# Kernel optimization log

Measured on AMD Instinct MI355X. Metric: run time of the kernel, lower is better.

The kernel has to match this reference:

```python
import jax, jax.numpy as jnp
import numpy as np

DIM = 512
HEADS = 8
HD = DIM // HEADS

def _rotate_half(t):
    t1, t2 = jnp.split(t, 2, axis=-1)
    return jnp.concatenate((-t2, t1), axis=-1)

def _layernorm(x, g, b, eps=1e-5):
    mu = jnp.mean(x, axis=-1, keepdims=True)
    var = jnp.var(x, axis=-1, keepdims=True)
    return (x - mu) * jax.lax.rsqrt(var + eps) * g + b

def setup_inputs() -> dict:
    key = jax.random.key(0)
    ks = jax.random.split(key, 12)
    B, S = 4, 2048
    x = jax.random.normal(ks[0], (B, S, DIM), dtype=jnp.float32)
    rope_cos = jax.random.uniform(ks[1], (1, S, 1, HD), dtype=jnp.float32)
    rope_sin = jax.random.uniform(ks[2], (1, S, 1, HD), dtype=jnp.float32)
    sd = 1.0 / np.sqrt(DIM)
    params = {
        'norm1_g': jnp.ones((DIM,), jnp.float32),
        'norm1_b': jnp.zeros((DIM,), jnp.float32),
        'norm2_g': jnp.ones((DIM,), jnp.float32),
        'norm2_b': jnp.zeros((DIM,), jnp.float32),
        'w_qkv': jax.random.uniform(ks[3], (DIM, 3 * DIM), jnp.float32, -sd, sd),
        'b_qkv': jax.random.uniform(ks[4], (3 * DIM,), jnp.float32, -sd, sd),
        'w_proj': jax.random.uniform(ks[5], (DIM, DIM), jnp.float32, -sd, sd),
        'b_proj': jax.random.uniform(ks[6], (DIM,), jnp.float32, -sd, sd),
        'w_fc1': jax.random.uniform(ks[7], (DIM, 4 * DIM), jnp.float32, -sd, sd),
        'b_fc1': jax.random.uniform(ks[8], (4 * DIM,), jnp.float32, -sd, sd),
        'w_fc2': jax.random.uniform(ks[9], (4 * DIM, DIM), jnp.float32, -1.0 / np.sqrt(4 * DIM), 1.0 / np.sqrt(4 * DIM)),
        'b_fc2': jax.random.uniform(ks[10], (DIM,), jnp.float32, -1.0 / np.sqrt(4 * DIM), 1.0 / np.sqrt(4 * DIM)),
    }
    return {'x': x, 'rope_cos': rope_cos, 'rope_sin': rope_sin, **params}

def reference(x, rope_cos, rope_sin, norm1_g, norm1_b, norm2_g, norm2_b,
              w_qkv, b_qkv, w_proj, b_proj, w_fc1, b_fc1, w_fc2, b_fc2):
    B, S, D = x.shape
    scale = 1.0 / np.sqrt(HD)
    shortcut = x
    h = _layernorm(x, norm1_g, norm1_b)
    qkv = (h @ w_qkv + b_qkv).reshape(B, S, 3, HEADS, HD)
    q, k, v = qkv[:, :, 0], qkv[:, :, 1], qkv[:, :, 2]  # [B,S,H,hd]
    q = q * rope_cos + _rotate_half(q) * rope_sin
    k = k * rope_cos + _rotate_half(k) * rope_sin
    # attention over heads: scores [B,H,S,S]
    attn = jnp.einsum('bqhd,bkhd->bhqk', q, k) * scale
    attn = jax.nn.softmax(attn, axis=-1)
    o = jnp.einsum('bhqk,bkhd->bqhd', attn, v).reshape(B, S, D)
    o = o @ w_proj + b_proj
    x = shortcut + o  # dropout is identity in eval
    h2 = _layernorm(x, norm2_g, norm2_b)
    mlp = jax.nn.gelu(h2 @ w_fc1 + b_fc1, approximate=False) @ w_fc2 + b_fc2
    return x + mlp
```

## Files before the change

kernel.cpp:

```cpp
#include <hip/hip_runtime.h>
#include <cstdint>
#include <cstddef>

typedef unsigned short u16;
typedef unsigned int   u32;
typedef __bf16 bf16x8 __attribute__((ext_vector_type(8)));
typedef float  f32x4  __attribute__((ext_vector_type(4)));

#define BS   8192
#define DIMM 512
#define NH   8
#define HD   64
#define SEQ  2048
#define DFF  2048
#define NQKV 1536

#define GLD16(g, l) __builtin_amdgcn_global_load_lds( \
    (__attribute__((address_space(1))) const void*)(g), \
    (__attribute__((address_space(3))) void*)(l), 16, 0, 0)

__device__ __forceinline__ float b2f(u16 s) {
  u32 u = ((u32)s) << 16;
  float f; __builtin_memcpy(&f, &u, 4); return f;
}
__device__ __forceinline__ u16 f2b(float f) {
  u32 u; __builtin_memcpy(&u, &f, 4);
  u += 0x7fffu + ((u >> 16) & 1u);
  return (u16)(u >> 16);
}
__device__ __forceinline__ u16 f2b_rtz(float f) {
  u32 u; __builtin_memcpy(&u, &f, 4);
  return (u16)(u >> 16);
}

#define SZ_QKV (DIMM * NQKV)
#define SZ_PRJ (DIMM * DIMM)
#define SZ_F1  (DIMM * DFF)
#define SZ_F2  (DFF * DIMM)
__global__ __launch_bounds__(256) void transpose_all_k(
    const float* __restrict__ w_qkv, const float* __restrict__ w_prj,
    const float* __restrict__ w_f1,  const float* __restrict__ w_f2,
    u16* __restrict__ o_qkv, u16* __restrict__ o_prj,
    u16* __restrict__ o_f1,  u16* __restrict__ o_f2) {
  int idx = blockIdx.x * 256 + threadIdx.x;
  const float* W; u16* O; int Kd, Nd, off;
  if (idx < SZ_QKV)                         { W = w_qkv; O = o_qkv; Kd = DIMM; Nd = NQKV; off = idx; }
  else if (idx < SZ_QKV + SZ_PRJ)           { W = w_prj; O = o_prj; Kd = DIMM; Nd = DIMM; off = idx - SZ_QKV; }
  else if (idx < SZ_QKV + SZ_PRJ + SZ_F1)   { W = w_f1;  O = o_f1;  Kd = DIMM; Nd = DFF;  off = idx - SZ_QKV - SZ_PRJ; }
  else                                      { W = w_f2;  O = o_f2;  Kd = DFF;  Nd = DIMM; off = idx - SZ_QKV - SZ_PRJ - SZ_F1; }
  int n = off / Kd, k = off - n * Kd;
  O[off] = f2b(W[(size_t)k * Nd + n]);
}

__global__ __launch_bounds__(256) void ln_f32b_k(const float* __restrict__ X,
    const float* __restrict__ G, const float* __restrict__ Bb, u16* __restrict__ out) {
  int w = threadIdx.x >> 6, lane = threadIdx.x & 63;
  size_t row = (size_t)blockIdx.x * 4 + w;
  const float* xr = X + row * DIMM;
  float v[8];
  *(float4*)&v[0] = *(const float4*)(xr + lane * 8);
  *(float4*)&v[4] = *(const float4*)(xr + lane * 8 + 4);
  float s = 0.f, s2 = 0.f;
#pragma unroll
  for (int j = 0; j < 8; j++) { s += v[j]; s2 += v[j] * v[j]; }
#pragma unroll
  for (int m = 1; m < 64; m <<= 1) { s += __shfl_xor(s, m); s2 += __shfl_xor(s2, m); }
  float mu = s * (1.f / DIMM);
  float rsd = rsqrtf(s2 * (1.f / DIMM) - mu * mu + 1e-5f);
  float g[8], bb[8];
  *(float4*)&g[0]  = *(const float4*)(G + lane * 8);
  *(float4*)&g[4]  = *(const float4*)(G + lane * 8 + 4);
  *(float4*)&bb[0] = *(const float4*)(Bb + lane * 8);
  *(float4*)&bb[4] = *(const float4*)(Bb + lane * 8 + 4);
  uint4 ov; u16* os = (u16*)&ov;
#pragma unroll
  for (int j = 0; j < 8; j++) os[j] = f2b((v[j] - mu) * rsd * g[j] + bb[j]);
  *(uint4*)(out + row * DIMM + lane * 8) = ov;
}

template <int EPI, int TM, int TN, int BK>
__global__ __launch_bounds__(256) void gemm_bt(const u16* __restrict__ A,
    const u16* __restrict__ BT, const float* __restrict__ bias,
    void* __restrict__ Cout, const float* __restrict__ resid, int N, int Kd) {
  constexpr int CPR  = BK / 8;
  constexpr int CPRB = (BK == 64) ? 3 : 2;
  constexpr int RS   = (BK == 64) ? 0 : 1;
  constexpr int KK   = BK / 32;
  constexpr int WROWS = (TN == 128) ? TM / 2 : TM / 4;
  constexpr int MT   = WROWS / 16;
  __shared__ __align__(16) u16 a_s[2][TM * BK];
  __shared__ __align__(16) u16 b_s[2][TN * BK];
  int t = threadIdx.x, lane = t & 63, w = t >> 6;
  int l15 = lane & 15, quad = lane >> 4;
  int gx = gridDim.x;
  int lid = blockIdx.x + gx * blockIdx.y;
  int per = (gx * gridDim.y) >> 3;
  int nid = (lid & 7) * per + (lid >> 3);
  int bx = nid % gx, by = nid / gx;
  int m0 = by * TM, n0 = bx * TN;
  int wm = (TN == 128) ? (w >> 1) * WROWS : w * WROWS;
  int wn = (TN == 128) ? (w & 1) * 64 : 0;
  f32x4 z4 = {0.f, 0.f, 0.f, 0.f};
  f32x4 acc[MT][4];
#pragma unroll
  for (int i = 0; i < MT; i++)
#pragma unroll
    for (int j = 0; j < 4; j++) acc[i][j] = z4;

#define GSTAGE(buf, ts) do {                                                  \
    int k0_ = (ts) * BK;                                                      \
    _Pragma("unroll")                                                         \
    for (int i = 0; i < TM * CPR / 256; i++) {                                \
      int c_ = t + i * 256;                                                   \
      int row_ = c_ >> CPRB, pos_ = c_ & (CPR - 1);                           \
      int ch_ = (pos_ ^ (row_ >> RS)) & (CPR - 1);                            \
      GLD16(A + (size_t)(m0 + row_) * Kd + k0_ + ch_ * 8, &a_s[buf][c_ * 8]); \
    }                                                                         \
    _Pragma("unroll")                                                         \
    for (int i = 0; i < TN * CPR / 256; i++) {                                \
      int c_ = t + i * 256;                                                   \
      int row_ = c_ >> CPRB, pos_ = c_ & (CPR - 1);                           \
      int ch_ = (pos_ ^ (row_ >> RS)) & (CPR - 1);                            \
      GLD16(BT + (size_t)(n0 + row_) * Kd + k0_ + ch_ * 8, &b_s[buf][c_ * 8]);\
    }                                                                         \
  } while (0)

#define GCOMPUTE(buf) do {                                                    \
    bf16x8 af[MT][KK], bfm[4][KK];                                            \
    _Pragma("unroll")                                                         \
    for (int mt = 0; mt < MT; mt++) {                                         \
      _Pragma("unroll")                                                       \
      for (int kk = 0; kk < KK; kk++) {                                       \
        int row_ = wm + mt * 16 + l15;                                        \
        int pos_ = ((kk * 4 + quad) ^ (row_ >> RS)) & (CPR - 1);              \
        af[mt][kk] = *(const bf16x8*)&a_s[buf][row_ * BK + pos_ * 8];         \
      }                                                                       \
    }                                                                         \
    _Pragma("unroll")                                                         \
    for (int nt = 0; nt < 4; nt++) {                                          \
      _Pragma("unroll")                                                       \
      for (int kk = 0; kk < KK; kk++) {                                       \
        int row_ = wn + nt * 16 + l15;                                        \
        int pos_ = ((kk * 4 + quad) ^ (row_ >> RS)) & (CPR - 1);              \
        bfm[nt][kk] = *(const bf16x8*)&b_s[buf][row_ * BK + pos_ * 8];        \
      }                                                                       \
    }                                                                         \
    _Pragma("unroll")                                                         \
    for (int kk = 0; kk < KK; kk++)                                           \
      _Pragma("unroll")                                                       \
      for (int mt = 0; mt < MT; mt++)                                         \
        _Pragma("unroll")                                                     \
        for (int nt = 0; nt < 4; nt++)                                        \
          acc[mt][nt] = __builtin_amdgcn_mfma_f32_16x16x32_bf16(              \
              af[mt][kk], bfm[nt][kk], acc[mt][nt], 0, 0, 0);                 \
  } while (0)

  GSTAGE(0, 0);
  __syncthreads();
  int nsteps = Kd / BK;
  for (int ts = 0; ts < nsteps; ts += 2) {
    GSTAGE(1, ts + 1);
    GCOMPUTE(0);
    __syncthreads();
    if (ts + 2 < nsteps) GSTAGE(0, ts + 2);
    GCOMPUTE(1);
    __syncthreads();
  }
#undef GSTAGE
#undef GCOMPUTE

#pragma unroll
  for (int nt = 0; nt < 4; nt++) {
    int col = n0 + wn + nt * 16 + l15;
    float bv = bias[col];
#pragma unroll
    for (int mt = 0; mt < MT; mt++) {
#pragma unroll
      for (int r = 0; r < 4; r++) {
        int rw = m0 + wm + mt * 16 + quad * 4 + r;
        float v = acc[mt][nt][r] + bv;
        size_t off = (size_t)rw * N + col;
        if (EPI == 0) {
          ((float*)Cout)[off] = v;
        } else if (EPI == 1) {
          ((float*)Cout)[off] = v + resid[off];
        } else if (EPI == 2) {
          ((u16*)Cout)[off] = f2b(0.5f * v * (1.f + erff(v * 0.70710678118654752f)));
        } else {
          ((u16*)Cout)[off] = f2b(v);
        }
      }
    }
  }
}

#define QSCALE 0.18033688f
__global__ __launch_bounds__(256) void rope_k(const u16* __restrict__ qkv,
    const float* __restrict__ C, const float* __restrict__ Sn,
    u16* __restrict__ Qo, u16* __restrict__ Ko, u16* __restrict__ Vo) {
  int idx = blockIdx.x * 256 + threadIdx.x;
  int row = idx / 192;
  int cn = idx - row * 192;
  int n0 = cn * 8;
  int comp = n0 >> 9;
  int hh = (n0 >> 6) & 7;
  int d0 = n0 & 63;
  int b = row >> 11, s = row & 2047;
  const u16* src = qkv + (size_t)row * NQKV;
  uint4 val = *(const uint4*)(src + n0);
  u16* vs = (u16*)&val;
  size_t oo = ((size_t)((b << 3) + hh) * SEQ + s) * HD + d0;
  if (comp == 2) { *(uint4*)(Vo + oo) = val; return; }
  uint4 pv = *(const uint4*)(src + (n0 ^ 32));
  u16* ps = (u16*)&pv;
  float cv[8], sv[8];
  *(float4*)&cv[0] = *(const float4*)(C + s * HD + d0);
  *(float4*)&cv[4] = *(const float4*)(C + s * HD + d0 + 4);
  *(float4*)&sv[0] = *(const float4*)(Sn + s * HD + d0);
  *(float4*)&sv[4] = *(const float4*)(Sn + s * HD + d0 + 4);
  float sgn = (d0 & 32) ? 1.f : -1.f;
  float sc = (comp == 0) ? QSCALE : 1.f;
  uint4 ov; u16* os = (u16*)&ov;
#pragma unroll
  for (int j = 0; j < 8; j++)
    os[j] = f2b(sc * (b2f(vs[j]) * cv[j] + sgn * b2f(ps[j]) * sv[j]));
  *(uint4*)((comp == 0 ? Qo : Ko) + oo) = ov;
}

__global__ __launch_bounds__(256) void vtrans_k(const u16* __restrict__ V,
                                                u16* __restrict__ Vt) {
  __shared__ u16 ld[64 * 72];
  int t = threadIdx.x;
  int bh = blockIdx.x >> 5;
  int s0 = (blockIdx.x & 31) * 64;
  const u16* src = V + (size_t)bh * SEQ * HD + (size_t)s0 * HD;
  u16* dst = Vt + (size_t)bh * SEQ * HD;
#pragma unroll
  for (int i = 0; i < 2; i++) {
    int c = t + i * 256, s = c >> 3, cp = c & 7;
    *(uint4*)&ld[s * 72 + ((cp ^ (s >> 3)) << 3)] =
        *(const uint4*)(src + (size_t)s * HD + cp * 8);
  }
  __syncthreads();
#pragma unroll
  for (int i = 0; i < 2; i++) {
    int c = t + i * 256, d = c >> 3, sc = c & 7;
    uint4 ov; u16* os = (u16*)&ov;
#pragma unroll
    for (int j = 0; j < 8; j++) {
      int s = sc * 8 + j;
      os[j] = ld[s * 72 + (((d >> 3) ^ (s >> 3)) << 3) + (d & 7)];
    }
    *(uint4*)(dst + (size_t)d * SEQ + s0 + sc * 8) = ov;
  }
}

__global__ __launch_bounds__(512) void attn_flash_k(const u16* __restrict__ Qg,
    const u16* __restrict__ Kg, const u16* __restrict__ Vtg, u16* __restrict__ Og) {
  __shared__ u16 q_s[128 * 72];
  __shared__ u16 k_s[64 * 72];
  __shared__ u16 vt_s[64 * 72];
  int t = threadIdx.x, lane = t & 63, w = t >> 6;
  int l15 = lane & 15, quad = lane >> 4;
  int lid = blockIdx.x;
  int nid = (lid & 7) * 64 + (lid >> 3);
  int bh = nid >> 4;
  int qt0 = (nid & 15) * 128;
  int b = bh >> 3, h = bh & 7;
  const u16* Qp = Qg + (size_t)bh * SEQ * HD;
  const u16* Kp = Kg + (size_t)bh * SEQ * HD;
  const u16* Vp = Vtg + (size_t)bh * SEQ * HD;
  int row = t >> 3, ch = t & 7;

  int sW = (w * 4 + quad) & 7;
  int pcol[4];
#pragma unroll
  for (int n = 0; n < 4; n++)
    pcol[n] = (((n * 2 + (l15 >> 3)) ^ sW) << 3) + (l15 & 7);
  int sR = (w * 4 + (l15 >> 2)) & 7;
  int pch[2];
#pragma unroll
  for (int kk = 0; kk < 2; kk++)
    pch[kk] = ((kk * 4 + quad) ^ sR) << 3;

#pragma unroll
  for (int i = 0; i < 2; i++) {
    int c = t + i * 512, qr = c >> 3, qc = c & 7;
    *(uint4*)&q_s[qr * 72 + qc * 8] = *(const uint4*)(Qp + (size_t)(qt0 + qr) * HD + qc * 8);
  }
  uint4 kr = *(const uint4*)(Kp + (size_t)row * HD + ch * 8);
  uint4 vr = *(const uint4*)(Vp + (size_t)row * SEQ + ch * 8);
  __syncthreads();
  bf16x8 qa[2];
  qa[0] = *(const bf16x8*)&q_s[(w * 16 + l15) * 72 + quad * 8];
  qa[1] = *(const bf16x8*)&q_s[(w * 16 + l15) * 72 + 32 + quad * 8];
  u16* p_s = q_s;
  f32x4 z4 = {0.f, 0.f, 0.f, 0.f};
  f32x4 of[4];
#pragma unroll
  for (int n = 0; n < 4; n++) of[n] = z4;
  float lrun[4] = {};

  for (int kt = 0; kt < SEQ; kt += 64) {
    __syncthreads();
    *(uint4*)&k_s[row * 72 + ch * 8] = kr;
    *(uint4*)&vt_s[row * 72 + ch * 8] = vr;
    __syncthreads();
    if (kt + 64 < SEQ) {
      kr = *(const uint4*)(Kp + (size_t)(kt + 64 + row) * HD + ch * 8);
      vr = *(const uint4*)(Vp + (size_t)row * SEQ + kt + 64 + ch * 8);
    }
    f32x4 sf[4];
#pragma unroll
    for (int n = 0; n < 4; n++) sf[n] = z4;
    __builtin_amdgcn_s_setprio(1);
#pragma unroll
    for (int kk = 0; kk < 2; kk++)
#pragma unroll
      for (int n = 0; n < 4; n++) {
        bf16x8 kb = *(const bf16x8*)&k_s[(n * 16 + l15) * 72 + kk * 32 + quad * 8];
        sf[n] = __builtin_amdgcn_mfma_f32_16x16x32_bf16(qa[kk], kb, sf[n], 0, 0, 0);
      }
    __builtin_amdgcn_s_setprio(0);
#pragma unroll
    for (int r = 0; r < 4; r++) {
      int prow = (w * 16 + quad * 4 + r) * 72;
#pragma unroll
      for (int n = 0; n < 4; n++) {
        float pp = exp2f(sf[n][r]);
        lrun[r] += pp;
        p_s[prow + pcol[n]] = f2b_rtz(pp);
      }
    }
    __builtin_amdgcn_s_setprio(1);
#pragma unroll
    for (int kk = 0; kk < 2; kk++) {
      bf16x8 pa = *(const bf16x8*)&p_s[(w * 16 + l15) * 72 + pch[kk]];
#pragma unroll
      for (int n = 0; n < 4; n++) {
        bf16x8 vb = *(const bf16x8*)&vt_s[(n * 16 + l15) * 72 + kk * 32 + quad * 8];
        of[n] = __builtin_amdgcn_mfma_f32_16x16x32_bf16(pa, vb, of[n], 0, 0, 0);
      }
    }
    __builtin_amdgcn_s_setprio(0);
  }
#pragma unroll
  for (int r = 0; r < 4; r++) {
    float l = lrun[r];
#pragma unroll
    for (int m = 1; m < 16; m <<= 1) l += __shfl_xor(l, m);
    float inv = 1.f / l;
    size_t orow = (size_t)(b * SEQ + qt0 + w * 16 + quad * 4 + r);
#pragma unroll
    for (int n = 0; n < 4; n++)
      Og[orow * DIMM + h * HD + n * 16 + l15] = f2b(of[n][r] * inv);
  }
}

extern "C" void kernel_launch(void* const* d_in, const int* in_sizes, int n_in,
                              void* d_out, int out_size, void* d_ws, size_t ws_size,
                              hipStream_t stream) {
  const float* x    = (const float*)d_in[0];
  const float* rc   = (const float*)d_in[1];
  const float* rsn  = (const float*)d_in[2];
  const float* n1g  = (const float*)d_in[3];
  const float* n1b  = (const float*)d_in[4];
  const float* n2g  = (const float*)d_in[5];
  const float* n2b  = (const float*)d_in[6];
  const float* wqkv = (const float*)d_in[7];
  const float* bqkv = (const float*)d_in[8];
  const float* wprj = (const float*)d_in[9];
  const float* bprj = (const float*)d_in[10];
  const float* wf1  = (const float*)d_in[11];
  const float* bf1  = (const float*)d_in[12];
  const float* wf2  = (const float*)d_in[13];
  const float* bf2  = (const float*)d_in[14];

  char* p = (char*)d_ws;
  u16*   wqkvT = (u16*)p;
  u16*   wprjT = (u16*)(p + (2u  << 20));
  u16*   wf1T  = (u16*)(p + (3u  << 20));
  u16*   wf2T  = (u16*)(p + (5u  << 20));
  u16*   h1    = (u16*)(p + (8u  << 20));
  u16*   qkvb  = (u16*)(p + (16u << 20));
  u16*   Vt    = (u16*)(p + (40u << 20));
  u16*   Qb    = (u16*)(p + (64u << 20));
  u16*   Kb    = (u16*)(p + (72u << 20));
  u16*   Vb    = (u16*)(p + (80u << 20));
  float* x2    = (float*)(p + (88u << 20));
  u16*   ob    = h1;
  u16*   h2    = h1;
  u16*   mid   = qkvb;

  transpose_all_k<<<dim3((SZ_QKV + SZ_PRJ + SZ_F1 + SZ_F2) / 256), 256, 0, stream>>>(
      wqkv, wprj, wf1, wf2, wqkvT, wprjT, wf1T, wf2T);

  ln_f32b_k<<<dim3(BS / 4), 256, 0, stream>>>(x, n1g, n1b, h1);

  gemm_bt<3, 64, 128, 32><<<dim3(NQKV / 128, BS / 64), 256, 0, stream>>>(h1, wqkvT, bqkv, qkvb, nullptr, NQKV, DIMM);

  rope_k<<<dim3(BS * NQKV / 8 / 256), 256, 0, stream>>>(qkvb, rc, rsn, Qb, Kb, Vb);

  vtrans_k<<<dim3(32 * (SEQ / 64)), 256, 0, stream>>>(Vb, Vt);

  attn_flash_k<<<dim3(32 * (SEQ / 128)), 512, 0, stream>>>(Qb, Kb, Vt, ob);

  gemm_bt<1, 64, 64, 64><<<dim3(DIMM / 64, BS / 64), 256, 0, stream>>>(ob, wprjT, bprj, x2, x, DIMM, DIMM);

  ln_f32b_k<<<dim3(BS / 4), 256, 0, stream>>>(x2, n2g, n2b, h2);

  gemm_bt<2, 64, 128, 32><<<dim3(DFF / 128, BS / 64), 256, 0, stream>>>(h2, wf1T, bf1, mid, nullptr, DFF, DIMM);

  gemm_bt<1, 64, 64, 64><<<dim3(DIMM / 64, BS / 64), 256, 0, stream>>>(mid, wf2T, bf2, (float*)d_out, x2, DIMM, DFF);
}
```

Baseline: 299.3 us.

## Fuse RoPE into QKV GEMM epilogue and double-buffer K/V tiles in attention

Removes the separate rope_k kernel by applying bias, RoPE, Q scaling and head-major scatter directly in the QKV GEMM epilogue, using the partner column held by the same wave (nt^2). This drops the round trip of the bf16 qkv intermediate through global memory, but the epilogue now writes scalar u16 values, which is less coalesced. The flash-attention kernel also double-buffers the K and Vt shared tiles so one barrier per iteration replaces two, at the cost of more LDS.

```diff
diff --git a/kernel.cpp b/kernel.cpp
--- a/kernel.cpp
+++ b/kernel.cpp
@@ -14,6 +14,7 @@
 #define SEQ  2048
 #define DFF  2048
 #define NQKV 1536
+#define QSCALE 0.18033688f
 
 #define GLD16(g, l) __builtin_amdgcn_global_load_lds( \
     (__attribute__((address_space(1))) const void*)(g), \
@@ -81,7 +82,9 @@
 template <int EPI, int TM, int TN, int BK>
 __global__ __launch_bounds__(256) void gemm_bt(const u16* __restrict__ A,
     const u16* __restrict__ BT, const float* __restrict__ bias,
-    void* __restrict__ Cout, const float* __restrict__ resid, int N, int Kd) {
+    void* __restrict__ Cout, const float* __restrict__ resid, int N, int Kd,
+    const float* __restrict__ rC, const float* __restrict__ rS,
+    u16* __restrict__ Qo, u16* __restrict__ Ko, u16* __restrict__ Vo) {
   constexpr int CPR  = BK / 8;
   constexpr int CPRB = (BK == 64) ? 3 : 2;
   constexpr int RS   = (BK == 64) ? 0 : 1;
@@ -169,6 +172,37 @@
 #undef GSTAGE
 #undef GCOMPUTE
 
+  if (EPI == 4) {
+    float bv4[4];
+#pragma unroll
+    for (int nt = 0; nt < 4; nt++) bv4[nt] = bias[n0 + wn + nt * 16 + l15];
+#pragma unroll
+    for (int nt = 0; nt < 4; nt++) {
+      int col = n0 + wn + nt * 16 + l15;
+      int comp = col >> 9, h = (col >> 6) & 7, d = col & 63;
+#pragma unroll
+      for (int mt = 0; mt < MT; mt++) {
+#pragma unroll
+        for (int r = 0; r < 4; r++) {
+          int rw = m0 + wm + mt * 16 + quad * 4 + r;
+          int bb_ = rw >> 11, s = rw & 2047;
+          float v = acc[mt][nt][r] + bv4[nt];
+          size_t oo = ((size_t)((bb_ << 3) + h) * SEQ + s) * HD + d;
+          if (comp == 2) {
+            Vo[oo] = f2b(v);
+          } else {
+            float pv = acc[mt][nt ^ 2][r] + bv4[nt ^ 2];
+            float cf = rC[(s << 6) + d], sf_ = rS[(s << 6) + d];
+            float sgn = (nt & 2) ? 1.f : -1.f;
+            float sc = (comp == 0) ? QSCALE : 1.f;
+            (comp == 0 ? Qo : Ko)[oo] = f2b(sc * (v * cf + sgn * pv * sf_));
+          }
+        }
+      }
+    }
+    return;
+  }
+
 #pragma unroll
   for (int nt = 0; nt < 4; nt++) {
     int col = n0 + wn + nt * 16 + l15;
@@ -194,39 +228,6 @@
   }
 }
 
-#define QSCALE 0.18033688f
-__global__ __launch_bounds__(256) void rope_k(const u16* __restrict__ qkv,
-    const float* __restrict__ C, const float* __restrict__ Sn,
-    u16* __restrict__ Qo, u16* __restrict__ Ko, u16* __restrict__ Vo) {
-  int idx = blockIdx.x * 256 + threadIdx.x;
-  int row = idx / 192;
-  int cn = idx - row * 192;
-  int n0 = cn * 8;
-  int comp = n0 >> 9;
-  int hh = (n0 >> 6) & 7;
-  int d0 = n0 & 63;
-  int b = row >> 11, s = row & 2047;
-  const u16* src = qkv + (size_t)row * NQKV;
-  uint4 val = *(const uint4*)(src + n0);
-  u16* vs = (u16*)&val;
-  size_t oo = ((size_t)((b << 3) + hh) * SEQ + s) * HD + d0;
-  if (comp == 2) { *(uint4*)(Vo + oo) = val; return; }
-  uint4 pv = *(const uint4*)(src + (n0 ^ 32));
-  u16* ps = (u16*)&pv;
-  float cv[8], sv[8];
-  *(float4*)&cv[0] = *(const float4*)(C + s * HD + d0);
-  *(float4*)&cv[4] = *(const float4*)(C + s * HD + d0 + 4);
-  *(float4*)&sv[0] = *(const float4*)(Sn + s * HD + d0);
-  *(float4*)&sv[4] = *(const float4*)(Sn + s * HD + d0 + 4);
-  float sgn = (d0 & 32) ? 1.f : -1.f;
-  float sc = (comp == 0) ? QSCALE : 1.f;
-  uint4 ov; u16* os = (u16*)&ov;
-#pragma unroll
-  for (int j = 0; j < 8; j++)
-    os[j] = f2b(sc * (b2f(vs[j]) * cv[j] + sgn * b2f(ps[j]) * sv[j]));
-  *(uint4*)((comp == 0 ? Qo : Ko) + oo) = ov;
-}
-
 __global__ __launch_bounds__(256) void vtrans_k(const u16* __restrict__ V,
                                                 u16* __restrict__ Vt) {
   __shared__ u16 ld[64 * 72];
@@ -258,8 +259,8 @@
 __global__ __launch_bounds__(512) void attn_flash_k(const u16* __restrict__ Qg,
     const u16* __restrict__ Kg, const u16* __restrict__ Vtg, u16* __restrict__ Og) {
   __shared__ u16 q_s[128 * 72];
-  __shared__ u16 k_s[64 * 72];
-  __shared__ u16 vt_s[64 * 72];
+  __shared__ u16 k_s[2][64 * 72];
+  __shared__ u16 vt_s[2][64 * 72];
   int t = threadIdx.x, lane = t & 63, w = t >> 6;
   int l15 = lane & 15, quad = lane >> 4;
   int lid = blockIdx.x;
@@ -290,6 +291,10 @@
   }
   uint4 kr = *(const uint4*)(Kp + (size_t)row * HD + ch * 8);
   uint4 vr = *(const uint4*)(Vp + (size_t)row * SEQ + ch * 8);
+  *(uint4*)&k_s[0][row * 72 + ch * 8] = kr;
+  *(uint4*)&vt_s[0][row * 72 + ch * 8] = vr;
+  kr = *(const uint4*)(Kp + (size_t)(64 + row) * HD + ch * 8);
+  vr = *(const uint4*)(Vp + (size_t)row * SEQ + 64 + ch * 8);
   __syncthreads();
   bf16x8 qa[2];
   qa[0] = *(const bf16x8*)&q_s[(w * 16 + l15) * 72 + quad * 8];
@@ -302,14 +307,7 @@
   float lrun[4] = {};
 
   for (int kt = 0; kt < SEQ; kt += 64) {
-    __syncthreads();
-    *(uint4*)&k_s[row * 72 + ch * 8] = kr;
-    *(uint4*)&vt_s[row * 72 + ch * 8] = vr;
-    __syncthreads();
-    if (kt + 64 < SEQ) {
-      kr = *(const uint4*)(Kp + (size_t)(kt + 64 + row) * HD + ch * 8);
-      vr = *(const uint4*)(Vp + (size_t)row * SEQ + kt + 64 + ch * 8);
-    }
+    int cur = (kt >> 6) & 1;
     f32x4 sf[4];
 #pragma unroll
     for (int n = 0; n < 4; n++) sf[n] = z4;
@@ -318,7 +316,7 @@
     for (int kk = 0; kk < 2; kk++)
 #pragma unroll
       for (int n = 0; n < 4; n++) {
-        bf16x8 kb = *(const bf16x8*)&k_s[(n * 16 + l15) * 72 + kk * 32 + quad * 8];
+        bf16x8 kb = *(const bf16x8*)&k_s[cur][(n * 16 + l15) * 72 + kk * 32 + quad * 8];
         sf[n] = __builtin_amdgcn_mfma_f32_16x16x32_bf16(qa[kk], kb, sf[n], 0, 0, 0);
       }
     __builtin_amdgcn_s_setprio(0);
@@ -338,11 +336,20 @@
       bf16x8 pa = *(const bf16x8*)&p_s[(w * 16 + l15) * 72 + pch[kk]];
 #pragma unroll
       for (int n = 0; n < 4; n++) {
-        bf16x8 vb = *(const bf16x8*)&vt_s[(n * 16 + l15) * 72 + kk * 32 + quad * 8];
+        bf16x8 vb = *(const bf16x8*)&vt_s[cur][(n * 16 + l15) * 72 + kk * 32 + quad * 8];
         of[n] = __builtin_amdgcn_mfma_f32_16x16x32_bf16(pa, vb, of[n], 0, 0, 0);
       }
     }
     __builtin_amdgcn_s_setprio(0);
+    if (kt + 64 < SEQ) {
+      *(uint4*)&k_s[cur ^ 1][row * 72 + ch * 8] = kr;
+      *(uint4*)&vt_s[cur ^ 1][row * 72 + ch * 8] = vr;
+      if (kt + 128 < SEQ) {
+        kr = *(const uint4*)(Kp + (size_t)(kt + 128 + row) * HD + ch * 8);
+        vr = *(const uint4*)(Vp + (size_t)row * SEQ + kt + 128 + ch * 8);
+      }
+    }
+    __syncthreads();
   }
 #pragma unroll
   for (int r = 0; r < 4; r++) {
@@ -382,34 +389,35 @@
   u16*   wf1T  = (u16*)(p + (3u  << 20));
   u16*   wf2T  = (u16*)(p + (5u  << 20));
   u16*   h1    = (u16*)(p + (8u  << 20));
-  u16*   qkvb  = (u16*)(p + (16u << 20));
-  u16*   Vt    = (u16*)(p + (40u << 20));
+  u16*   mid   = (u16*)(p + (16u << 20));
+  u16*   Vt    = (u16*)(p + (48u << 20));
   u16*   Qb    = (u16*)(p + (64u << 20));
   u16*   Kb    = (u16*)(p + (72u << 20));
   u16*   Vb    = (u16*)(p + (80u << 20));
   float* x2    = (float*)(p + (88u << 20));
   u16*   ob    = h1;
   u16*   h2    = h1;
-  u16*   mid   = qkvb;
 
   transpose_all_k<<<dim3((SZ_QKV + SZ_PRJ + SZ_F1 + SZ_F2) / 256), 256, 0, stream>>>(
       wqkv, wprj, wf1, wf2, wqkvT, wprjT, wf1T, wf2T);
 
   ln_f32b_k<<<dim3(BS / 4), 256, 0, stream>>>(x, n1g, n1b, h1);
 
-  gemm_bt<3, 64, 128, 32><<<dim3(NQKV / 128, BS / 64), 256, 0, stream>>>(h1, wqkvT, bqkv, qkvb, nullptr, NQKV, DIMM);
-
-  rope_k<<<dim3(BS * NQKV / 8 / 256), 256, 0, stream>>>(qkvb, rc, rsn, Qb, Kb, Vb);
+  gemm_bt<4, 64, 128, 32><<<dim3(NQKV / 128, BS / 64), 256, 0, stream>>>(
+      h1, wqkvT, bqkv, nullptr, nullptr, NQKV, DIMM, rc, rsn, Qb, Kb, Vb);
 
   vtrans_k<<<dim3(32 * (SEQ / 64)), 256, 0, stream>>>(Vb, Vt);
 
   attn_flash_k<<<dim3(32 * (SEQ / 128)), 512, 0, stream>>>(Qb, Kb, Vt, ob);
 
-  gemm_bt<1, 64, 64, 64><<<dim3(DIMM / 64, BS / 64), 256, 0, stream>>>(ob, wprjT, bprj, x2, x, DIMM, DIMM);
+  gemm_bt<1, 64, 64, 64><<<dim3(DIMM / 64, BS / 64), 256, 0, stream>>>(
+      ob, wprjT, bprj, x2, x, DIMM, DIMM, nullptr, nullptr, nullptr, nullptr, nullptr);
 
   ln_f32b_k<<<dim3(BS / 4), 256, 0, stream>>>(x2, n2g, n2b, h2);
 
-  gemm_bt<2, 64, 128, 32><<<dim3(DFF / 128, BS / 64), 256, 0, stream>>>(h2, wf1T, bf1, mid, nullptr, DFF, DIMM);
-
-  gemm_bt<1, 64, 64, 64><<<dim3(DIMM / 64, BS / 64), 256, 0, stream>>>(mid, wf2T, bf2, (float*)d_out, x2, DIMM, DFF);
-}
+  gemm_bt<2, 64, 128, 32><<<dim3(DFF / 128, BS / 64), 256, 0, stream>>>(
+      h2, wf1T, bf1, mid, nullptr, DFF, DIMM, nullptr, nullptr, nullptr, nullptr, nullptr);
+
+  gemm_bt<1, 64, 64, 64><<<dim3(DIMM / 64, BS / 64), 256, 0, stream>>>(
+      mid, wf2T, bf2, (float*)d_out, x2, DIMM, DFF, nullptr, nullptr, nullptr, nullptr, nullptr);
+}
```

New measurement: 312.4 us. +4.4%, slower.
